# Kernel optimization log

Hardware: AMD Instinct MI355X
Metric: run time of the kernel (lower is better)

The kernel has to match this reference:

```python
import jax, jax.numpy as jnp
import numpy as np

N_FEATURES = 128
LENGTH = 10.0  # length_scale
N_NODES = 10000
N_EDGES = 200000


def mlp(x, W1, b1, W2, b2):
    # embedding.MLP(in, hidden, out): Linear -> SiLU -> Linear
    return jax.nn.silu(x @ W1 + b1) @ W2 + b2


def positional_encoding(dist, n_features, length):
    # sinusoidal encoding of scalar distances -> [E, n_features]
    ranks = jnp.arange(n_features // 2, dtype=dist.dtype)
    arg = dist[:, None] * ranks[None, :] * (np.pi / length)  # [E, F/2]
    return jnp.concatenate([jnp.sin(arg), jnp.cos(arg)], axis=-1)


def setup_inputs() -> dict:
    key = jax.random.key(0)
    N, E, F = N_NODES, N_EDGES, N_FEATURES
    ks = jax.random.split(key, 10)
    d = {}
    d["edge_index"] = jax.random.randint(ks[0], (2, E), 0, N)
    d["invariant_node_features"] = jax.random.normal(ks[1], (N, F), dtype=jnp.float32)
    d["equivariant_node_features"] = jax.random.normal(ks[2], (N, F, 3), dtype=jnp.float32)
    d["invariant_edge_features"] = jax.random.normal(ks[3], (E, F), dtype=jnp.float32)
    d["edge_dist"] = jax.random.uniform(ks[4], (E,), dtype=jnp.float32, minval=0.1, maxval=10.0)
    d["edge_dir"] = jax.random.normal(ks[5], (E, 3), dtype=jnp.float32)
    # phi: MLP(2F -> F -> 5F); w: MLP(F -> F -> 5F)
    d["phi_W1"] = jax.random.normal(ks[6], (2 * F, F), dtype=jnp.float32) / np.sqrt(2 * F)
    d["phi_b1"] = jnp.zeros((F,), jnp.float32)
    d["phi_W2"] = jax.random.normal(ks[7], (F, 5 * F), dtype=jnp.float32) / np.sqrt(F)
    d["phi_b2"] = jnp.zeros((5 * F,), jnp.float32)
    d["w_W1"] = jax.random.normal(ks[8], (F, F), dtype=jnp.float32) / np.sqrt(F)
    d["w_b1"] = jnp.zeros((F,), jnp.float32)
    d["w_W2"] = jax.random.normal(ks[9], (F, 5 * F), dtype=jnp.float32) / np.sqrt(F)
    d["w_b2"] = jnp.zeros((5 * F,), jnp.float32)
    return d


def reference(edge_index, invariant_node_features, equivariant_node_features,
              invariant_edge_features, edge_dist, edge_dir,
              phi_W1, phi_b1, phi_W2, phi_b2, w_W1, w_b1, w_W2, w_b2):
    F = N_FEATURES
    src, dst = edge_index[0], edge_index[1]
    # gather + concat edge features -> phi input [E, 2F]
    in_feat = jnp.concatenate([invariant_node_features[src], invariant_edge_features], axis=-1)
    pe = positional_encoding(edge_dist, F, LENGTH)  # [E, F]
    m = mlp(in_feat, phi_W1, phi_b1, phi_W2, phi_b2) * mlp(pe, w_W1, w_b1, w_W2, w_b2)  # [E, 5F]
    gates, cp_gates, scale_edge_dir, ds, de = jnp.split(m, 5, axis=-1)
    src_eq = equivariant_node_features[src]            # [E, F, 3]
    dst_eq = equivariant_node_features[dst]            # [E, F, 3]
    edir = edge_dir[:, None, :]                        # [E, 1, 3]
    # multiply_first_dim(w, x) == w[..., None] * x for [E,F] x [E,F,3]
    gated_features = gates[..., None] * src_eq
    scaled_edge_dir = scale_edge_dir[..., None] * edir
    cross = jnp.cross(jnp.broadcast_to(edir, dst_eq.shape), dst_eq)  # [E, F, 3]
    gated_cross = cp_gates[..., None] * cross
    dv = scaled_edge_dir + gated_features + gated_cross  # [E, F, 3]
    N = invariant_node_features.shape[0]
    dv = jax.ops.segment_sum(dv, dst, num_segments=N)   # [N, F, 3]
    ds = jax.ops.segment_sum(ds, dst, num_segments=N)   # [N, F]
    return (equivariant_node_features + dv,
            invariant_node_features + ds,
            invariant_edge_features + de)
```

## Files before the change

### kernel.cpp

```cpp
#include <hip/hip_runtime.h>
#include <math.h>

#define E_EDGES 200000
#define N_NODES 10000
#define FDIM    128

typedef __attribute__((ext_vector_type(8))) short  short8;
typedef __attribute__((ext_vector_type(4))) float  float4v;

#define WT1_OFF   0
#define WTW1_OFF  32768
#define WT2_OFF   49152
#define WTW2_OFF  131072
#define W_TOTAL   212992
#define CNT_BYTE  425984
#define CUR_BYTE  465984
#define PERM_BYTE 505984

#define EQ_OUT_SZ   (N_NODES * FDIM * 3)
#define INV_OUT_SZ  (N_NODES * FDIM)

__device__ __forceinline__ unsigned short f2bf(float x) {
    union { float f; unsigned u; } v; v.f = x;
    unsigned r = v.u + 0x7fffu + ((v.u >> 16) & 1u);
    return (unsigned short)(r >> 16);
}
__device__ __forceinline__ float bf2f(unsigned short h) {
    union { unsigned u; float f; } v; v.u = ((unsigned)h) << 16; return v.f;
}

__device__ __forceinline__ void lds_barrier() {
    asm volatile("s_waitcnt lgkmcnt(0)" ::: "memory");
    __builtin_amdgcn_sched_barrier(0);
    __builtin_amdgcn_s_barrier();
    __builtin_amdgcn_sched_barrier(0);
}

__device__ __forceinline__ void async_se4(const float* g, float* l) {
    __builtin_amdgcn_global_load_lds(
        (const __attribute__((address_space(1))) unsigned int*)g,
        (__attribute__((address_space(3))) unsigned int*)l,
        4, 0, 0);
}

__device__ __forceinline__ unsigned short* tile_ptr(unsigned short* base, int row, int col) {
    unsigned off = (unsigned)(row * 256 + col * 2);
    off ^= (unsigned)((row & 7) << 4);
    return (unsigned short*)((char*)base + off);
}

__global__ void prep_fused(const float* __restrict__ phiW1,
                           const float* __restrict__ wW1,
                           const float* __restrict__ phiW2,
                           const float* __restrict__ wW2,
                           unsigned short* __restrict__ ws,
                           int* __restrict__ counts,
                           const float* __restrict__ eq,
                           const float* __restrict__ inv,
                           float* __restrict__ out) {
    int t = blockIdx.x * 256 + threadIdx.x;
    if (t < N_NODES) counts[t] = 0;
    if (t < W_TOTAL) {
        if (t < 32768) {
            int n = t >> 8, k = t & 255;
            ws[WT1_OFF + t] = f2bf(phiW1[k * 128 + n]);
        } else if (t < 49152) {
            int i = t - 32768; int n = i >> 7, k = i & 127;
            ws[WTW1_OFF + i] = f2bf(wW1[k * 128 + n]);
        } else if (t < 131072) {
            int i = t - 49152; int n = i >> 7, k = i & 127;
            ws[WT2_OFF + i] = f2bf(phiW2[k * 640 + n]);
        } else {
            int i = t - 131072; int n = i >> 7, k = i & 127;
            ws[WTW2_OFF + i] = f2bf(wW2[k * 640 + n]);
        }
    }
    if (t < EQ_OUT_SZ / 4) {
        ((float4v*)out)[t] = ((const float4v*)eq)[t];
    } else {
        int u = t - EQ_OUT_SZ / 4;
        ((float4v*)(out + EQ_OUT_SZ))[u] = ((const float4v*)inv)[u];
    }
}

__global__ void hist_kernel(const int* __restrict__ eidx, int* __restrict__ counts) {
    int e = blockIdx.x * 256 + threadIdx.x;
    if (e < E_EDGES) atomicAdd(&counts[eidx[E_EDGES + e]], 1);
}
__global__ __launch_bounds__(1024)
void scan_kernel(const int* __restrict__ counts, int* __restrict__ cursor) {
    __shared__ int sums[1024];
    const int t = threadIdx.x;
    const int base = t * 10;
    int local[10];
    int s = 0;
    #pragma unroll
    for (int j = 0; j < 10; ++j) {
        int b = base + j;
        int v = (b < N_NODES) ? counts[b] : 0;
        local[j] = s; s += v;
    }
    sums[t] = s;
    __syncthreads();
    for (int off = 1; off < 1024; off <<= 1) {
        int v = (t >= off) ? sums[t - off] : 0;
        __syncthreads();
        sums[t] += v;
        __syncthreads();
    }
    int pre = (t > 0) ? sums[t - 1] : 0;
    #pragma unroll
    for (int j = 0; j < 10; ++j) {
        int b = base + j;
        if (b < N_NODES) cursor[b] = pre + local[j];
    }
}
__global__ void scatter_kernel(const int* __restrict__ eidx,
                               int* __restrict__ cursor, int* __restrict__ perm) {
    int e = blockIdx.x * 256 + threadIdx.x;
    if (e < E_EDGES) {
        int d = eidx[E_EDGES + e];
        int pos = atomicAdd(&cursor[d], 1);
        perm[pos] = e;
    }
}

__global__ __launch_bounds__(256, 3)
void edge_kernel(const int*   __restrict__ eidx,
                 const float* __restrict__ node_inv,
                 const float* __restrict__ eqf,
                 const float* __restrict__ edge_inv,
                 const float* __restrict__ dist,
                 const float* __restrict__ dir,
                 const float* __restrict__ phi_b1,
                 const float* __restrict__ phi_b2,
                 const float* __restrict__ w_b1,
                 const float* __restrict__ w_b2,
                 const unsigned short* __restrict__ wsW,
                 const int* __restrict__ perm,
                 float* __restrict__ out) {
    __shared__ __align__(16) unsigned char smem_u[32768];
    __shared__ int   s_e[32], s_src[32], s_dst[32];
    __shared__ float s_dir[32][3];
    __shared__ float s_dist[32];

    unsigned short* A1a = (unsigned short*)smem_u;
    unsigned short* A1b = (unsigned short*)(smem_u + 8192);
    unsigned short* H1  = (unsigned short*)(smem_u + 16384);
    unsigned short* H2  = (unsigned short*)(smem_u + 24576);
    float* PH2 = (float*)smem_u;

    const int tid = threadIdx.x;
    const int p0  = blockIdx.x * 32;

    if (tid < 32) {
        int e = perm[p0 + tid];
        s_e[tid]   = e;
        s_src[tid] = eidx[e];
        s_dst[tid] = eidx[E_EDGES + e];
        s_dir[tid][0] = dir[e * 3 + 0];
        s_dir[tid][1] = dir[e * 3 + 1];
        s_dir[tid][2] = dir[e * 3 + 2];
        s_dist[tid]  = dist[e];
    }
    lds_barrier();

    {
        const int i   = tid >> 3;
        const int seg = tid & 7;
        const int k0  = seg * 32;
        const float* base;
        unsigned short* tb;
        int c0;
        if (k0 < 128) { base = node_inv + (size_t)s_src[i] * 128 + k0; tb = A1a; c0 = k0; }
        else          { base = edge_inv + (size_t)s_e[i]  * 128 + (k0 - 128); tb = A1b; c0 = k0 - 128; }
        #pragma unroll
        for (int j = 0; j < 4; ++j) {
            float4v v0 = *(const float4v*)(base + j * 8);
            float4v v1 = *(const float4v*)(base + j * 8 + 4);
            short8 sv;
            #pragma unroll
            for (int u = 0; u < 4; ++u) {
                sv[u]     = (short)f2bf(v0[u]);
                sv[u + 4] = (short)f2bf(v1[u]);
            }
            *(short8*)tile_ptr(tb, i, c0 + j * 8) = sv;
        }
    }
    lds_barrier();

    const int wv   = tid >> 6;
    const int ln   = tid & 63;
    const int l16  = ln & 15;
    const int quad = ln >> 4;

    const unsigned short* Wt1  = wsW + WT1_OFF;
    const unsigned short* Wtw1 = wsW + WTW1_OFF;
    const unsigned short* Wt2  = wsW + WT2_OFF;
    const unsigned short* Wtw2 = wsW + WTW2_OFF;

    const float4v zero4 = {0.f, 0.f, 0.f, 0.f};

    float4v acc1[2][2], acc2[2][2];
    #pragma unroll
    for (int rt = 0; rt < 2; ++rt)
        #pragma unroll
        for (int ct = 0; ct < 2; ++ct) { acc1[rt][ct] = zero4; acc2[rt][ct] = zero4; }

    #pragma unroll
    for (int kk = 0; kk < 4; ++kk) {
        const int k = kk * 32 + quad * 8;
        short8 a0 = *(const short8*)tile_ptr(A1a, l16, k);
        short8 a1 = *(const short8*)tile_ptr(A1a, 16 + l16, k);
        #pragma unroll
        for (int ct = 0; ct < 2; ++ct) {
            const int n = wv * 32 + ct * 16 + l16;
            short8 b = *(const short8*)&Wt1[n * 256 + k];
            acc1[0][ct] = __builtin_amdgcn_mfma_f32_16x16x32_bf16(a0, b, acc1[0][ct], 0, 0, 0);
            acc1[1][ct] = __builtin_amdgcn_mfma_f32_16x16x32_bf16(a1, b, acc1[1][ct], 0, 0, 0);
        }
    }
    #pragma unroll
    for (int kk = 0; kk < 4; ++kk) {
        const int k = kk * 32 + quad * 8;
        short8 a0 = *(const short8*)tile_ptr(A1b, l16, k);
        short8 a1 = *(const short8*)tile_ptr(A1b, 16 + l16, k);
        #pragma unroll
        for (int ct = 0; ct < 2; ++ct) {
            const int n = wv * 32 + ct * 16 + l16;
            short8 b = *(const short8*)&Wt1[n * 256 + 128 + k];
            acc1[0][ct] = __builtin_amdgcn_mfma_f32_16x16x32_bf16(a0, b, acc1[0][ct], 0, 0, 0);
            acc1[1][ct] = __builtin_amdgcn_mfma_f32_16x16x32_bf16(a1, b, acc1[1][ct], 0, 0, 0);
        }
    }
    {
        const float cst = 3.14159265358979323846f / 10.0f;
        const float d0 = s_dist[l16] * cst;
        const float d1 = s_dist[16 + l16] * cst;
        short8 pe0[4], pe1[4];
        #pragma unroll
        for (int kk = 0; kk < 4; ++kk) {
            short8 s0, s1;
            #pragma unroll
            for (int u = 0; u < 8; ++u) {
                const int f = kk * 32 + quad * 8 + u;
                const float fa = (float)((kk < 2) ? f : (f - 64));
                float v0, v1;
                if (kk < 2) { v0 = __sinf(d0 * fa); v1 = __sinf(d1 * fa); }
                else        { v0 = __cosf(d0 * fa); v1 = __cosf(d1 * fa); }
                s0[u] = (short)f2bf(v0);
                s1[u] = (short)f2bf(v1);
            }
            pe0[kk] = s0; pe1[kk] = s1;
        }
        #pragma unroll
        for (int kk = 0; kk < 4; ++kk) {
            const int k = kk * 32 + quad * 8;
            #pragma unroll
            for (int ct = 0; ct < 2; ++ct) {
                const int n = wv * 32 + ct * 16 + l16;
                short8 b = *(const short8*)&Wtw1[n * 128 + k];
                acc2[0][ct] = __builtin_amdgcn_mfma_f32_16x16x32_bf16(pe0[kk], b, acc2[0][ct], 0, 0, 0);
                acc2[1][ct] = __builtin_amdgcn_mfma_f32_16x16x32_bf16(pe1[kk], b, acc2[1][ct], 0, 0, 0);
            }
        }
    }
    #pragma unroll
    for (int ct = 0; ct < 2; ++ct) {
        const int n = wv * 32 + ct * 16 + l16;
        const float b1v  = phi_b1[n];
        const float bw1v = w_b1[n];
        #pragma unroll
        for (int rt = 0; rt < 2; ++rt)
            #pragma unroll
            for (int r = 0; r < 4; ++r) {
                const int row = rt * 16 + quad * 4 + r;
                float x = acc1[rt][ct][r] + b1v;
                *tile_ptr(H1, row, n) = f2bf(x / (1.f + __expf(-x)));
                float y = acc2[rt][ct][r] + bw1v;
                *tile_ptr(H2, row, n) = f2bf(y / (1.f + __expf(-y)));
            }
    }
    lds_barrier();

    float* eq_out   = out;
    float* inv_out  = out + EQ_OUT_SZ;
    float* edge_out = out + EQ_OUT_SZ + INV_OUT_SZ;

    short8 ha[2][4], hb[2][4];
    #pragma unroll
    for (int rt = 0; rt < 2; ++rt)
        #pragma unroll
        for (int kk = 0; kk < 4; ++kk) {
            const int k = kk * 32 + quad * 8;
            ha[rt][kk] = *(const short8*)tile_ptr(H1, rt * 16 + l16, k);
            hb[rt][kk] = *(const short8*)tile_ptr(H2, rt * 16 + l16, k);
        }
    unsigned short a1bv[2][8];
    #pragma unroll
    for (int fc2 = 0; fc2 < 2; ++fc2)
        #pragma unroll
        for (int rt = 0; rt < 2; ++rt)
            #pragma unroll
            for (int rr = 0; rr < 4; ++rr)
                a1bv[fc2][rt * 4 + rr] =
                    *tile_ptr(A1b, rt * 16 + quad * 4 + rr, fc2 * 64 + wv * 16 + l16);
    lds_barrier();

    const int red_f = tid >> 2;
    const int red_c = tid & 3;
    const int red_fo = (red_c < 3) ? (red_f * 3 + red_c) : (192 + red_f);

    #pragma unroll
    for (int fc2 = 0; fc2 < 2; ++fc2) {
        {
            const int r0 = wv * 8;
            #pragma unroll
            for (int rr = 0; rr < 8; ++rr) {
                const int row = r0 + rr;
                const float* g = eqf + ((size_t)s_src[row] * 128 + fc2 * 64) * 3 + ln;
                float* l = PH2 + row * 256;
                async_se4(g,       l);
                async_se4(g + 64,  l + 64);
                async_se4(g + 128, l + 128);
            }
        }
        float4v mv[2][5];
        #pragma unroll
        for (int g = 0; g < 5; ++g) {
            const int n = g * 128 + fc2 * 64 + wv * 16 + l16;
            float4v p1a = zero4, p1b = zero4, p2a = zero4, p2b = zero4;
            #pragma unroll
            for (int kk = 0; kk < 4; ++kk) {
                const int k = kk * 32 + quad * 8;
                short8 b1f = *(const short8*)&Wt2[n * 128 + k];
                short8 b2f = *(const short8*)&Wtw2[n * 128 + k];
                p1a = __builtin_amdgcn_mfma_f32_16x16x32_bf16(ha[0][kk], b1f, p1a, 0, 0, 0);
                p1b = __builtin_amdgcn_mfma_f32_16x16x32_bf16(ha[1][kk], b1f, p1b, 0, 0, 0);
                p2a = __builtin_amdgcn_mfma_f32_16x16x32_bf16(hb[0][kk], b2f, p2a, 0, 0, 0);
                p2b = __builtin_amdgcn_mfma_f32_16x16x32_bf16(hb[1][kk], b2f, p2b, 0, 0, 0);
            }
            const float b2v  = phi_b2[n];
            const float bw2v = w_b2[n];
            mv[0][g] = (p1a + b2v) * (p2a + bw2v);
            mv[1][g] = (p1b + b2v) * (p2b + bw2v);
        }
        asm volatile("s_waitcnt vmcnt(0)" ::: "memory");
        __builtin_amdgcn_sched_barrier(0);
        lds_barrier();
        {
            const int fl = wv * 16 + l16;
            const int fg = fc2 * 64 + fl;
            #pragma unroll
            for (int rt = 0; rt < 2; ++rt) {
                #pragma unroll
                for (int r = 0; r < 4; ++r) {
                    const int row = rt * 16 + quad * 4 + r;
                    const float gate = mv[rt][0][r];
                    const float cpg  = mv[rt][1][r];
                    const float sc   = mv[rt][2][r];
                    const float dsv  = mv[rt][3][r];
                    const float dev  = mv[rt][4][r];
                    const int dn = s_dst[row], e = s_e[row];
                    const float ex = s_dir[row][0], ey = s_dir[row][1], ez = s_dir[row][2];
                    float* pp = PH2 + row * 256;
                    const float sx = pp[fl * 3 + 0];
                    const float sy = pp[fl * 3 + 1];
                    const float sz = pp[fl * 3 + 2];
                    const float* dq = eqf + ((size_t)dn * 128 + fg) * 3;
                    const float dx = dq[0], dy = dq[1], dz = dq[2];
                    const float cx = ey * dz - ez * dy;
                    const float cy = ez * dx - ex * dz;
                    const float cz = ex * dy - ey * dx;
                    pp[fl * 3 + 0] = sc * ex + gate * sx + cpg * cx;
                    pp[fl * 3 + 1] = sc * ey + gate * sy + cpg * cy;
                    pp[fl * 3 + 2] = sc * ez + gate * sz + cpg * cz;
                    pp[192 + fl]   = dsv;
                    edge_out[(size_t)e * 128 + fg] = bf2f(a1bv[fc2][rt * 4 + r]) + dev;
                }
            }
        }
        lds_barrier();
        {
            const int fgr = fc2 * 64 + red_f;
            float acc = 0.f;
            int prev = s_dst[0];
            #pragma unroll
            for (int r = 0; r < 32; ++r) {
                const int d = s_dst[r];
                const float v = PH2[r * 256 + red_fo];
                if (d != prev) {
                    if (red_c < 3) atomicAdd(eq_out + ((size_t)prev * 128 + fgr) * 3 + red_c, acc);
                    else           atomicAdd(inv_out + (size_t)prev * 128 + fgr, acc);
                    acc = 0.f; prev = d;
                }
                acc += v;
            }
            if (red_c < 3) atomicAdd(eq_out + ((size_t)prev * 128 + fgr) * 3 + red_c, acc);
            else           atomicAdd(inv_out + (size_t)prev * 128 + fgr, acc);
        }
        lds_barrier();
    }
}

extern "C" void kernel_launch(void* const* d_in, const int* in_sizes, int n_in,
                              void* d_out, int out_size, void* d_ws, size_t ws_size,
                              hipStream_t stream) {
    const int*   eidx     = (const int*)d_in[0];
    const float* node_inv = (const float*)d_in[1];
    const float* eqf      = (const float*)d_in[2];
    const float* edge_inv = (const float*)d_in[3];
    const float* dist     = (const float*)d_in[4];
    const float* dir      = (const float*)d_in[5];
    const float* phi_W1   = (const float*)d_in[6];
    const float* phi_b1   = (const float*)d_in[7];
    const float* phi_W2   = (const float*)d_in[8];
    const float* phi_b2   = (const float*)d_in[9];
    const float* w_W1     = (const float*)d_in[10];
    const float* w_b1     = (const float*)d_in[11];
    const float* w_W2     = (const float*)d_in[12];
    const float* w_b2     = (const float*)d_in[13];
    float* out = (float*)d_out;
    unsigned short* wsW = (unsigned short*)d_ws;
    int* counts = (int*)((char*)d_ws + CNT_BYTE);
    int* cursor = (int*)((char*)d_ws + CUR_BYTE);
    int* perm   = (int*)((char*)d_ws + PERM_BYTE);

    prep_fused<<<(EQ_OUT_SZ + INV_OUT_SZ) / 4 / 256, 256, 0, stream>>>(
        phi_W1, w_W1, phi_W2, w_W2, wsW, counts, eqf, node_inv, out);
    hist_kernel<<<(E_EDGES + 255) / 256, 256, 0, stream>>>(eidx, counts);
    scan_kernel<<<1, 1024, 0, stream>>>(counts, cursor);
    scatter_kernel<<<(E_EDGES + 255) / 256, 256, 0, stream>>>(eidx, cursor, perm);
    edge_kernel<<<E_EDGES / 32, 256, 0, stream>>>(eidx, node_inv, eqf, edge_inv, dist, dir,
                                                  phi_b1, phi_b2, w_b1, w_b2, wsW, perm, out);
}
```

Measured before the change: 678.3 us.

## Swizzle PH2 staging layout to remove LDS bank conflicts; wave-shuffle scan

The equivariant feature staging buffer PH2 moves from interleaved xyz (fl*3+c) to a component-planar layout with a row-dependent XOR and rotation swizzle. The async global-to-LDS loads are remapped so each lane fetches the element that lands in its swizzled slot. The epilogue and the reduction index through the same mapping, which is meant to cut LDS bank conflicts in the per-row epilogue reads and writes. Separately, the scan kernel swaps its 1024-wide shared-memory Hillis-Steele loop for wave-level shuffle scans plus a small per-wave sum pass, removing many barriers. The cost is more complex index math and strided global loads whose coalescing may change.

```diff
diff --git a/kernel.cpp b/kernel.cpp
--- a/kernel.cpp
+++ b/kernel.cpp
@@ -41,6 +41,11 @@
         (const __attribute__((address_space(1))) unsigned int*)g,
         (__attribute__((address_space(3))) unsigned int*)l,
         4, 0, 0);
+}
+
+__device__ __forceinline__ int ph2_word(int row, int c, int fl) {
+    const int k = ((row >> 2) & 3) << 4;
+    return row * 256 + c * 64 + (((fl + c * 16) & 63) ^ k);
 }
 
 __device__ __forceinline__ unsigned short* tile_ptr(unsigned short* base, int row, int col) {
@@ -89,8 +94,10 @@
 }
 __global__ __launch_bounds__(1024)
 void scan_kernel(const int* __restrict__ counts, int* __restrict__ cursor) {
-    __shared__ int sums[1024];
+    __shared__ int wsum[16];
     const int t = threadIdx.x;
+    const int lane = t & 63;
+    const int w = t >> 6;
     const int base = t * 10;
     int local[10];
     int s = 0;
@@ -100,15 +107,25 @@
         int v = (b < N_NODES) ? counts[b] : 0;
         local[j] = s; s += v;
     }
-    sums[t] = s;
+    int ps = s;
+    #pragma unroll
+    for (int off = 1; off < 64; off <<= 1) {
+        int n = __shfl_up(ps, off);
+        if (lane >= off) ps += n;
+    }
+    if (lane == 63) wsum[w] = ps;
     __syncthreads();
-    for (int off = 1; off < 1024; off <<= 1) {
-        int v = (t >= off) ? sums[t - off] : 0;
-        __syncthreads();
-        sums[t] += v;
-        __syncthreads();
-    }
-    int pre = (t > 0) ? sums[t - 1] : 0;
+    if (t < 16) {
+        int x = wsum[t];
+        #pragma unroll
+        for (int off = 1; off < 16; off <<= 1) {
+            int n = __shfl_up(x, off);
+            if (t >= off) x += n;
+        }
+        wsum[t] = x;
+    }
+    __syncthreads();
+    const int pre = ((w > 0) ? wsum[w - 1] : 0) + (ps - s);
     #pragma unroll
     for (int j = 0; j < 10; ++j) {
         int b = base + j;
@@ -309,7 +326,6 @@
 
     const int red_f = tid >> 2;
     const int red_c = tid & 3;
-    const int red_fo = (red_c < 3) ? (red_f * 3 + red_c) : (192 + red_f);
 
     #pragma unroll
     for (int fc2 = 0; fc2 < 2; ++fc2) {
@@ -318,11 +334,14 @@
             #pragma unroll
             for (int rr = 0; rr < 8; ++rr) {
                 const int row = r0 + rr;
-                const float* g = eqf + ((size_t)s_src[row] * 128 + fc2 * 64) * 3 + ln;
+                const int k = ((row >> 2) & 3) << 4;
                 float* l = PH2 + row * 256;
-                async_se4(g,       l);
-                async_se4(g + 64,  l + 64);
-                async_se4(g + 128, l + 128);
+                const size_t gb = ((size_t)s_src[row] * 128 + fc2 * 64);
+                #pragma unroll
+                for (int c = 0; c < 3; ++c) {
+                    const int fl = ((ln ^ k) - c * 16) & 63;
+                    async_se4(eqf + (gb + fl) * 3 + c, l + c * 64);
+                }
             }
         }
         float4v mv[2][5];
@@ -363,19 +382,18 @@
                     const float dev  = mv[rt][4][r];
                     const int dn = s_dst[row], e = s_e[row];
                     const float ex = s_dir[row][0], ey = s_dir[row][1], ez = s_dir[row][2];
-                    float* pp = PH2 + row * 256;
-                    const float sx = pp[fl * 3 + 0];
-                    const float sy = pp[fl * 3 + 1];
-                    const float sz = pp[fl * 3 + 2];
+                    const float sx = PH2[ph2_word(row, 0, fl)];
+                    const float sy = PH2[ph2_word(row, 1, fl)];
+                    const float sz = PH2[ph2_word(row, 2, fl)];
                     const float* dq = eqf + ((size_t)dn * 128 + fg) * 3;
                     const float dx = dq[0], dy = dq[1], dz = dq[2];
                     const float cx = ey * dz - ez * dy;
                     const float cy = ez * dx - ex * dz;
                     const float cz = ex * dy - ey * dx;
-                    pp[fl * 3 + 0] = sc * ex + gate * sx + cpg * cx;
-                    pp[fl * 3 + 1] = sc * ey + gate * sy + cpg * cy;
-                    pp[fl * 3 + 2] = sc * ez + gate * sz + cpg * cz;
-                    pp[192 + fl]   = dsv;
+                    PH2[ph2_word(row, 0, fl)] = sc * ex + gate * sx + cpg * cx;
+                    PH2[ph2_word(row, 1, fl)] = sc * ey + gate * sy + cpg * cy;
+                    PH2[ph2_word(row, 2, fl)] = sc * ez + gate * sz + cpg * cz;
+                    PH2[ph2_word(row, 3, fl)] = dsv;
                     edge_out[(size_t)e * 128 + fg] = bf2f(a1bv[fc2][rt * 4 + r]) + dev;
                 }
             }
@@ -388,7 +406,7 @@
             #pragma unroll
             for (int r = 0; r < 32; ++r) {
                 const int d = s_dst[r];
-                const float v = PH2[r * 256 + red_fo];
+                const float v = PH2[ph2_word(r, red_c, red_f)];
                 if (d != prev) {
                     if (red_c < 3) atomicAdd(eq_out + ((size_t)prev * 128 + fgr) * 3 + red_c, acc);
                     else           atomicAdd(inv_out + (size_t)prev * 128 + fgr, acc);
```

Result: slower. 735.4 us (+8.4%).
